# Kernel tuning notes

Measured on AMD Instinct MI355X. Metric: run time of the kernel, lower is better.

The kernel has to match this reference:

```python
import jax, jax.numpy as jnp
import numpy as np

D_IN = 768      # residual-stream width
D_SAE = 16384   # dictionary size
T = 4           # positions per window
K = 64          # TopK sparsity
PREFIX = (8192, 16384)  # prefix_sum for n_scales=2 even split
B = 1024


def setup_inputs() -> dict:
    key = jax.random.key(0)
    ks = jax.random.split(key, 6)
    x = jax.random.normal(ks[0], (B, T, D_IN), jnp.float32)
    # encoder weight ~ kaiming-uniform scale
    W_enc = jax.random.normal(ks[1], (T, D_IN, D_SAE), jnp.float32) * (1.0 / np.sqrt(D_IN))
    b_enc = jnp.zeros((D_SAE,), jnp.float32)
    # per-scale decoders, row-normalized over (T, d_in) as in _normalize_decoder
    def make_dec(k, prefix):
        W = jax.random.normal(k, (prefix, T, D_IN), jnp.float32)
        norms = jnp.linalg.norm(W.reshape(prefix, -1), axis=1).clip(1e-8)
        return W / norms[:, None, None]
    W_dec0 = make_dec(ks[2], PREFIX[0])
    W_dec1 = make_dec(ks[3], PREFIX[1])
    b_dec0 = jnp.zeros((T, D_IN), jnp.float32)
    b_dec1 = jnp.zeros((T, D_IN), jnp.float32)
    # non-identity per-position prefix permutation (T, d_sae)
    perm_keys = jax.random.split(ks[4], T)
    pos_prefix_perm = jax.vmap(lambda k: jax.random.permutation(k, D_SAE))(perm_keys).astype(jnp.int32)
    return {
        'x': x, 'W_enc': W_enc, 'b_enc': b_enc,
        'W_dec0': W_dec0, 'b_dec0': b_dec0,
        'W_dec1': W_dec1, 'b_dec1': b_dec1,
        'pos_prefix_perm': pos_prefix_perm,
    }


def reference(x, W_enc, b_enc, W_dec0, b_dec0, W_dec1, b_dec1, pos_prefix_perm):
    # ---- encode: pre-activation + per-row TopK + ReLU scatter into sparse code z
    pre = jnp.einsum('btd,tds->bs', x, W_enc) + b_enc            # (B, d_sae)
    vals, idx = jax.lax.top_k(pre, K)                            # (B, K)
    b = pre.shape[0]
    z = jnp.zeros_like(pre).at[jnp.arange(b)[:, None], idx].set(jax.nn.relu(vals))
    # ---- matryoshka per-(position, scale) reconstruction loss
    total = jnp.asarray(0.0, pre.dtype)
    x_hat_full = None
    for W, bd in ((W_dec0, b_dec0), (W_dec1, b_dec1)):
        prefix = W.shape[0]
        # position-dependent permutation gather: z_g[b,t,p] = z[b, perm[t,p]]
        z_g = z[:, pos_prefix_perm[:, :prefix]]                  # (B, T, prefix)
        x_hat = jnp.einsum('btp,ptd->btd', z_g, W) + bd          # (B, T, d_in)
        # sum over t of mean_b sum_d err^2  (== loop over t in the original)
        total = total + jnp.sum(jnp.mean(jnp.sum((x_hat - x) ** 2, axis=-1), axis=0))
        x_hat_full = x_hat
    total = total / (T * 2)  # divide by T * n_scales
    # aux-k loss: freshly initialized module has no dead latents
    # (num_tokens_since_fired starts at 0 << dead_threshold_tokens), so l_auxk == 0.
    return total, x_hat_full, z
```

## Files before the change

### kernel.cpp

```cpp
#include <hip/hip_runtime.h>
#include <hip/hip_bf16.h>
#include <stdint.h>

#define NB    1024
#define NT    4
#define NDIN  768
#define NSAE  16384
#define NK    64
#define KDIM  3072
#define PFX0  8192
#define KT96  96
#define VKD   6144

typedef _Float16 f16x8 __attribute__((ext_vector_type(8)));
typedef _Float16 f16x4 __attribute__((ext_vector_type(4)));
typedef float    f32x4 __attribute__((ext_vector_type(4)));

__device__ __forceinline__ unsigned f2key(float f) {
    union { float f; unsigned u; } cv; cv.f = f;
    unsigned u = cv.u;
    return u ^ ((unsigned)((int)u >> 31) | 0x80000000u);
}

__device__ __forceinline__ void ld16(const void* g, void* l) {
    __builtin_amdgcn_global_load_lds(
        (const __attribute__((address_space(1))) void*)g,
        (__attribute__((address_space(3))) void*)l, 16, 0, 0);
}

__global__ __launch_bounds__(256) void conv_a_kernel(
    const float* __restrict__ A, _Float16* __restrict__ A2)
{
    const int gid = blockIdx.x * 256 + threadIdx.x;
    const int m = gid / (KDIM / 4);
    const int k = (gid % (KDIM / 4)) * 4;
    const float4 v = *(const float4*)(A + (size_t)m * KDIM + k);
    const float vv[4] = { v.x, v.y, v.z, v.w };
    f16x4 h, l;
#pragma unroll
    for (int j = 0; j < 4; ++j) {
        const float sv = vv[j] * 64.f;
        const _Float16 hh = (_Float16)sv;
        h[j] = hh;
        l[j] = (_Float16)(sv - (float)hh);
    }
    const size_t ob = (size_t)m * VKD + (k >> 5) * 64 + (k & 31);
    *(f16x4*)(A2 + ob)      = h;
    *(f16x4*)(A2 + ob + 32) = l;
}

__global__ __launch_bounds__(512, 2) void gemm_f16split_kernel(
    const _Float16* __restrict__ A2, const float* __restrict__ Bsrc,
    const float* __restrict__ bias, float* __restrict__ pre)
{
    __shared__ _Float16 sA[2 * 256 * 64];
    __shared__ float    sB32[32 * 256];
    __shared__ _Float16 sBf[256 * 64];
    const int tid = threadIdx.x;
    const int lane = tid & 63;
    const int wid = tid >> 6;
    const int wm = wid >> 2;
    const int wn = wid & 3;

    const int bid = blockIdx.x;
    const int swz = (bid & 7) * 32 + (bid >> 3);
    const int m0 = (swz & 3) * 256;
    const int n0 = (swz >> 2) * 256;

    const _Float16* pa[4]; const float* pb[4];
    _Float16* da[4]; float* db[4];
#pragma unroll
    for (int r = 0; r < 4; ++r) {
        const int d = tid + r * 512;
        const int rowA = d >> 3;
        const int lsA = (d & 7) ^ (rowA & 7);
        pa[r] = A2 + (size_t)(m0 + rowA) * VKD + lsA * 8;
        da[r] = sA + d * 8;
        const int kB = d >> 6;
        const int slotB = d & 63;
        pb[r] = Bsrc + (size_t)kB * NSAE + n0 + slotB * 4;
        db[r] = sB32 + d * 4;
    }

    const int rl = lane & 15;
    const int qw = lane >> 4;
    const int off0 = ((0 + qw) ^ (rl & 7)) * 8 + rl * 64;
    const int off1 = ((4 + qw) ^ (rl & 7)) * 8 + rl * 64;

    const int cvn = tid & 255;
    const int cvkh = tid >> 8;
    const int cvsw = cvn & 7;
    _Float16* const cvout = sBf + cvn * 64;

    f32x4 acc[8][4];
#pragma unroll
    for (int mi = 0; mi < 8; ++mi)
#pragma unroll
        for (int ni = 0; ni < 4; ++ni)
            acc[mi][ni] = (f32x4){0.f, 0.f, 0.f, 0.f};

#pragma unroll
    for (int r = 0; r < 4; ++r) { ld16(pa[r], da[r]); ld16(pb[r], db[r]); }
    asm volatile("s_waitcnt vmcnt(0)" ::: "memory");
    __builtin_amdgcn_sched_barrier(0);
    __builtin_amdgcn_s_barrier();
    __builtin_amdgcn_sched_barrier(0);

    const size_t KSTRB = (size_t)32 * NSAE;

    for (int kt = 0; kt < KT96; ++kt) {
        const int cbA = (kt & 1) ? 16384 : 0;
        const int nbA = cbA ^ 16384;

        {
            float v[16];
#pragma unroll
            for (int j = 0; j < 16; ++j)
                v[j] = sB32[(cvkh * 16 + j) * 256 + cvn];
            f16x8 h0{}, h1{}, l0{}, l1{};
#pragma unroll
            for (int j = 0; j < 8; ++j) {
                const float sv = v[j] * 64.f;
                const _Float16 hh = (_Float16)sv;
                h0[j] = hh;
                l0[j] = (_Float16)(sv - (float)hh);
            }
#pragma unroll
            for (int j = 0; j < 8; ++j) {
                const float sv = v[8 + j] * 64.f;
                const _Float16 hh = (_Float16)sv;
                h1[j] = hh;
                l1[j] = (_Float16)(sv - (float)hh);
            }
            *(f16x8*)(cvout + (((cvkh * 2 + 0) ^ cvsw) * 8)) = h0;
            *(f16x8*)(cvout + (((cvkh * 2 + 1) ^ cvsw) * 8)) = h1;
            *(f16x8*)(cvout + (((4 + cvkh * 2 + 0) ^ cvsw) * 8)) = l0;
            *(f16x8*)(cvout + (((4 + cvkh * 2 + 1) ^ cvsw) * 8)) = l1;
        }
        asm volatile("s_waitcnt lgkmcnt(0)" ::: "memory");
        __builtin_amdgcn_sched_barrier(0);
        __builtin_amdgcn_s_barrier();
        __builtin_amdgcn_sched_barrier(0);

        if (kt + 1 < KT96) {
            const int koA = (kt + 1) * 64;
            const size_t koB = (size_t)(kt + 1) * KSTRB;
#pragma unroll
            for (int r = 0; r < 4; ++r) {
                ld16(pa[r] + koA, da[r] + nbA);
                ld16(pb[r] + koB, db[r]);
            }
        }
        __builtin_amdgcn_s_setprio(1);
        f16x8 bf[4][2];
#pragma unroll
        for (int ni = 0; ni < 4; ++ni) {
            const int rb = (wn * 64 + ni * 16) * 64;
            bf[ni][0] = *(const f16x8*)(sBf + rb + off0);
            bf[ni][1] = *(const f16x8*)(sBf + rb + off1);
        }
#pragma unroll
        for (int h = 0; h < 2; ++h) {
            f16x8 af[4][2];
#pragma unroll
            for (int i = 0; i < 4; ++i) {
                const int ra = cbA + (wm * 128 + (h * 4 + i) * 16) * 64;
                af[i][0] = *(const f16x8*)(sA + ra + off0);
                af[i][1] = *(const f16x8*)(sA + ra + off1);
            }
#pragma unroll
            for (int i = 0; i < 4; ++i)
#pragma unroll
                for (int ni = 0; ni < 4; ++ni) {
                    acc[h * 4 + i][ni] = __builtin_amdgcn_mfma_f32_16x16x32_f16(af[i][0], bf[ni][0], acc[h * 4 + i][ni], 0, 0, 0);
                    acc[h * 4 + i][ni] = __builtin_amdgcn_mfma_f32_16x16x32_f16(af[i][0], bf[ni][1], acc[h * 4 + i][ni], 0, 0, 0);
                    acc[h * 4 + i][ni] = __builtin_amdgcn_mfma_f32_16x16x32_f16(af[i][1], bf[ni][0], acc[h * 4 + i][ni], 0, 0, 0);
                }
        }
        __builtin_amdgcn_s_setprio(0);
        __builtin_amdgcn_sched_barrier(0);
        asm volatile("s_waitcnt vmcnt(0)" ::: "memory");
        __builtin_amdgcn_sched_barrier(0);
        __builtin_amdgcn_s_barrier();
        __builtin_amdgcn_sched_barrier(0);
    }

    const float c12 = 1.0f / 4096.0f;
    float bv[4];
#pragma unroll
    for (int ni = 0; ni < 4; ++ni) bv[ni] = bias[n0 + wn * 64 + ni * 16 + rl];
#pragma unroll
    for (int mi = 0; mi < 8; ++mi)
#pragma unroll
        for (int ni = 0; ni < 4; ++ni)
#pragma unroll
            for (int r = 0; r < 4; ++r) {
                const int row = m0 + wm * 128 + mi * 16 + qw * 4 + r;
                const int col = n0 + wn * 64 + ni * 16 + rl;
                pre[(size_t)row * NSAE + col] = acc[mi][ni][r] * c12 + bv[ni];
            }
}

__global__ __launch_bounds__(256) void gemm_pre_kernel(
    const float* __restrict__ A, const float* __restrict__ Bm,
    const float* __restrict__ bias, float* __restrict__ pre)
{
    __shared__ float As[16][128];
    __shared__ float Bs[16][128];
    const int bn = blockIdx.x * 128;
    const int bm = blockIdx.y * 128;
    const int tid = threadIdx.x;
    const int tx = tid & 15;
    const int ty = tid >> 4;

    float acc[8][8];
#pragma unroll
    for (int i = 0; i < 8; ++i)
#pragma unroll
        for (int j = 0; j < 8; ++j) acc[i][j] = 0.f;

    for (int k0 = 0; k0 < KDIM; k0 += 16) {
#pragma unroll
        for (int i = 0; i < 2; ++i) {
            const int idx = i * 256 + tid;
            const int r = idx >> 2;
            const int c = (idx & 3) << 2;
            const float4 v = *(const float4*)(A + (size_t)(bm + r) * KDIM + (k0 + c));
            As[c + 0][r] = v.x; As[c + 1][r] = v.y;
            As[c + 2][r] = v.z; As[c + 3][r] = v.w;
        }
#pragma unroll
        for (int i = 0; i < 2; ++i) {
            const int idx = i * 256 + tid;
            const int r = idx >> 5;
            const int c = (idx & 31) << 2;
            *(float4*)(&Bs[r][c]) = *(const float4*)(Bm + (size_t)(k0 + r) * NSAE + (bn + c));
        }
        __syncthreads();
#pragma unroll
        for (int kk = 0; kk < 16; ++kk) {
            const float4 a0 = *(const float4*)(&As[kk][ty * 8]);
            const float4 a1 = *(const float4*)(&As[kk][ty * 8 + 4]);
            const float4 b0 = *(const float4*)(&Bs[kk][tx * 8]);
            const float4 b1 = *(const float4*)(&Bs[kk][tx * 8 + 4]);
            const float av[8] = { a0.x, a0.y, a0.z, a0.w, a1.x, a1.y, a1.z, a1.w };
            const float bv[8] = { b0.x, b0.y, b0.z, b0.w, b1.x, b1.y, b1.z, b1.w };
#pragma unroll
            for (int i = 0; i < 8; ++i)
#pragma unroll
                for (int j = 0; j < 8; ++j)
                    acc[i][j] = fmaf(av[i], bv[j], acc[i][j]);
        }
        __syncthreads();
    }

    float bv8[8];
#pragma unroll
    for (int j = 0; j < 8; ++j) bv8[j] = bias[bn + tx * 8 + j];
#pragma unroll
    for (int i = 0; i < 8; ++i) {
        float4 o0, o1;
        o0.x = acc[i][0] + bv8[0]; o0.y = acc[i][1] + bv8[1];
        o0.z = acc[i][2] + bv8[2]; o0.w = acc[i][3] + bv8[3];
        o1.x = acc[i][4] + bv8[4]; o1.y = acc[i][5] + bv8[5];
        o1.z = acc[i][6] + bv8[6]; o1.w = acc[i][7] + bv8[7];
        const size_t off = (size_t)(bm + ty * 8 + i) * NSAE + bn + tx * 8;
        *(float4*)(pre + off) = o0;
        *(float4*)(pre + off + 4) = o1;
    }
}

__global__ __launch_bounds__(256) void topk_kernel(
    const float* __restrict__ pre,
    int* __restrict__ tk_idx, float* __restrict__ tk_val,
    float* __restrict__ z)
{
    __shared__ unsigned hist[4][256];
    __shared__ int sel[NK];
    __shared__ float sval[NK];
    __shared__ int ties[256];
    __shared__ float tval[256];
    __shared__ unsigned sh_prefix, sh_want, sh_cnt, sh_tiecnt;

    const int b = blockIdx.x;
    const int tid = threadIdx.x;
    const int w = tid >> 6;
    const float* row = pre + (size_t)b * NSAE;
    float* zrow = z + (size_t)b * NSAE;

    if (tid == 0) { sh_prefix = 0u; sh_want = NK; sh_cnt = 0u; sh_tiecnt = 0u; }
    hist[0][tid] = 0u; hist[1][tid] = 0u; hist[2][tid] = 0u; hist[3][tid] = 0u;
    __syncthreads();

    float4 rv[16];
#pragma unroll
    for (int j = 0; j < 16; ++j) {
        const int i = tid * 4 + j * 1024;
        rv[j] = *(const float4*)(row + i);
        *(float4*)(zrow + i) = make_float4(0.f, 0.f, 0.f, 0.f);
        atomicAdd(&hist[w][f2key(rv[j].x) >> 24], 1u);
        atomicAdd(&hist[w][f2key(rv[j].y) >> 24], 1u);
        atomicAdd(&hist[w][f2key(rv[j].z) >> 24], 1u);
        atomicAdd(&hist[w][f2key(rv[j].w) >> 24], 1u);
    }
    __syncthreads();
    hist[0][tid] += hist[1][tid] + hist[2][tid] + hist[3][tid];
    __syncthreads();
    if (tid == 0) {
        unsigned cum = 0u; int bsel = 0;
        for (int bin = 255; bin >= 0; --bin) {
            const unsigned c = hist[0][bin];
            if (cum + c >= NK) { bsel = bin; break; }
            cum += c;
        }
        sh_prefix = ((unsigned)bsel << 24);
        sh_want = NK - cum;
    }
    __syncthreads();

    for (int pass = 1; pass < 4; ++pass) {
        hist[0][tid] = 0u; hist[1][tid] = 0u; hist[2][tid] = 0u; hist[3][tid] = 0u;
        __syncthreads();
        const int shift = 24 - pass * 8;
        const unsigned mask = 0xFFFFFFFFu << (shift + 8);
        const unsigned pfx = sh_prefix;
#pragma unroll
        for (int j = 0; j < 16; ++j) {
            const float fv[4] = { rv[j].x, rv[j].y, rv[j].z, rv[j].w };
#pragma unroll
            for (int q = 0; q < 4; ++q) {
                const unsigned k = f2key(fv[q]);
                if ((k & mask) == pfx) atomicAdd(&hist[w][(k >> shift) & 0xFFu], 1u);
            }
        }
        __syncthreads();
        hist[0][tid] += hist[1][tid] + hist[2][tid] + hist[3][tid];
        __syncthreads();
        if (tid == 0) {
            const unsigned want = sh_want;
            unsigned cum = 0u; int bsel = 0;
            for (int bin = 255; bin >= 0; --bin) {
                const unsigned c = hist[0][bin];
                if (cum + c >= want) { bsel = bin; break; }
                cum += c;
            }
            sh_prefix |= ((unsigned)bsel << shift);
            sh_want = want - cum;
        }
        __syncthreads();
    }

    const unsigned T = sh_prefix;
#pragma unroll
    for (int j = 0; j < 16; ++j) {
        const float fv[4] = { rv[j].x, rv[j].y, rv[j].z, rv[j].w };
#pragma unroll
        for (int q = 0; q < 4; ++q) {
            const unsigned k = f2key(fv[q]);
            if (k > T) {
                const unsigned s = atomicAdd(&sh_cnt, 1u);
                sel[s] = tid * 4 + j * 1024 + q;
                sval[s] = fv[q];
            } else if (k == T) {
                const unsigned s = atomicAdd(&sh_tiecnt, 1u);
                if (s < 256u) { ties[s] = tid * 4 + j * 1024 + q; tval[s] = fv[q]; }
            }
        }
    }
    __syncthreads();
    if (tid == 0) {
        const unsigned tc = sh_tiecnt;
        const int n = (int)(tc < 256u ? tc : 256u);
        for (int a = 1; a < n; ++a) {
            const int v = ties[a]; const float fv = tval[a]; int c = a;
            while (c > 0 && ties[c - 1] > v) {
                ties[c] = ties[c - 1]; tval[c] = tval[c - 1]; --c;
            }
            ties[c] = v; tval[c] = fv;
        }
        const int base = (int)sh_cnt;
        const int want = (int)sh_want;
        for (int j = 0; j < want && j < n; ++j) {
            sel[base + j] = ties[j]; sval[base + j] = tval[j];
        }
    }
    __syncthreads();
    if (tid < NK) {
        const int myi = sel[tid];
        int rank = 0;
#pragma unroll 1
        for (int j = 0; j < NK; ++j) rank += (sel[j] < myi) ? 1 : 0;
        const float v = fmaxf(sval[tid], 0.f);
        tk_idx[b * NK + rank] = myi;
        tk_val[b * NK + rank] = v;
        zrow[myi] = v;
    }
}

__global__ __launch_bounds__(256) void invperm_kernel(
    const int* __restrict__ perm, int* __restrict__ ipos)
{
    const int i = blockIdx.x * 256 + threadIdx.x;
    if (i < NT * NSAE) {
        const int t = i >> 14;
        ipos[t * NSAE + perm[i]] = i & (NSAE - 1);
    }
}

__global__ __launch_bounds__(256) void decode_kernel(
    const float* __restrict__ x,
    const int* __restrict__ tk_idx, const float* __restrict__ tk_val,
    const int* __restrict__ ipos,
    const float* __restrict__ Wd0, const float* __restrict__ bd0,
    const float* __restrict__ Wd1, const float* __restrict__ bd1,
    float* __restrict__ xhat, float* __restrict__ part0, float* __restrict__ part1)
{
    const int gbid = blockIdx.x;
    const int t = gbid >> 10;
    const int b = gbid & (NB - 1);
    const int bt = b * NT + t;
    const int tid = threadIdx.x;

    __shared__ int s_p[NK];
    __shared__ float s_v[NK];
    if (tid < NK) {
        const int s = tk_idx[b * NK + tid];
        s_v[tid] = tk_val[b * NK + tid];
        s_p[tid] = ipos[t * NSAE + s];
    }
    __syncthreads();

    float acc0[3], acc1[3];
#pragma unroll
    for (int r = 0; r < 3; ++r) {
        const int d = tid + 256 * r;
        acc0[r] = bd0[t * NDIN + d];
        acc1[r] = bd1[t * NDIN + d];
    }
    for (int j = 0; j < NK; ++j) {
        const int p = s_p[j];
        const float v = s_v[j];
        const float* w1 = Wd1 + ((size_t)p * NT + t) * NDIN;
#pragma unroll
        for (int r = 0; r < 3; ++r) acc1[r] = fmaf(v, w1[tid + 256 * r], acc1[r]);
        if (p < PFX0) {
            const float* w0 = Wd0 + ((size_t)p * NT + t) * NDIN;
#pragma unroll
            for (int r = 0; r < 3; ++r) acc0[r] = fmaf(v, w0[tid + 256 * r], acc0[r]);
        }
    }

    float e0 = 0.f, e1 = 0.f;
#pragma unroll
    for (int r = 0; r < 3; ++r) {
        const int d = tid + 256 * r;
        const float xv = x[(size_t)bt * NDIN + d];
        const float d0 = acc0[r] - xv;
        const float d1 = acc1[r] - xv;
        e0 = fmaf(d0, d0, e0);
        e1 = fmaf(d1, d1, e1);
        xhat[(size_t)bt * NDIN + d] = acc1[r];
    }

    __shared__ float r0[256];
    __shared__ float r1[256];
    r0[tid] = e0; r1[tid] = e1;
    __syncthreads();
    for (int w = 128; w > 0; w >>= 1) {
        if (tid < w) { r0[tid] += r0[tid + w]; r1[tid] += r1[tid + w]; }
        __syncthreads();
    }
    if (tid == 0) { part0[bt] = r0[0]; part1[bt] = r1[0]; }
}

__global__ __launch_bounds__(256) void reduce_kernel(
    const float* __restrict__ part0, const float* __restrict__ part1,
    float* __restrict__ out_total)
{
    __shared__ double red[256];
    const int tid = threadIdx.x;
    double s = 0.0;
    for (int i = tid; i < NB * NT; i += 256)
        s += (double)part0[i] + (double)part1[i];
    red[tid] = s;
    __syncthreads();
    for (int w = 128; w > 0; w >>= 1) {
        if (tid < w) red[tid] += red[tid + w];
        __syncthreads();
    }
    if (tid == 0) out_total[0] = (float)(red[0] / ((double)NB * (double)(NT * 2)));
}

extern "C" void kernel_launch(void* const* d_in, const int* in_sizes, int n_in,
                              void* d_out, int out_size, void* d_ws, size_t ws_size,
                              hipStream_t stream)
{
    const float* x     = (const float*)d_in[0];
    const float* W_enc = (const float*)d_in[1];
    const float* b_enc = (const float*)d_in[2];
    const float* Wd0   = (const float*)d_in[3];
    const float* bd0   = (const float*)d_in[4];
    const float* Wd1   = (const float*)d_in[5];
    const float* bd1   = (const float*)d_in[6];
    const int*   perm  = (const int*)d_in[7];

    float* out       = (float*)d_out;
    float* out_total = out;
    float* out_xhat  = out + 1;
    float* out_z     = out + 1 + (size_t)NB * NT * NDIN;

    char* ws = (char*)d_ws;
    size_t off = 0;
    float* pre = (float*)(ws + off); off += (size_t)NB * NSAE * sizeof(float);

    const size_t szA2 = (size_t)NB * VKD * sizeof(_Float16);
    _Float16* A2 = (_Float16*)(ws + off);
    const size_t off_splits_end = off + szA2;

    const bool fast = (ws_size >= off_splits_end +
        ((size_t)NB * NK * 8 + (size_t)NT * NSAE * 4 + (size_t)NB * NT * 8));
    size_t tail = fast ? off_splits_end : off;
    int*   tk_idx = (int*)(ws + tail);   tail += (size_t)NB * NK * sizeof(int);
    float* tk_val = (float*)(ws + tail); tail += (size_t)NB * NK * sizeof(float);
    int*   ipos   = (int*)(ws + tail);   tail += (size_t)NT * NSAE * sizeof(int);
    float* part0  = (float*)(ws + tail); tail += (size_t)NB * NT * sizeof(float);
    float* part1  = (float*)(ws + tail);

    if (fast) {
        conv_a_kernel<<<(NB * KDIM) / (256 * 4), 256, 0, stream>>>(x, A2);
        gemm_f16split_kernel<<<256, 512, 0, stream>>>(A2, W_enc, b_enc, pre);
    } else {
        gemm_pre_kernel<<<dim3(NSAE / 128, NB / 128), 256, 0, stream>>>(x, W_enc, b_enc, pre);
    }
    invperm_kernel<<<(NT * NSAE) / 256, 256, 0, stream>>>(perm, ipos);
    topk_kernel<<<NB, 256, 0, stream>>>(pre, tk_idx, tk_val, out_z);
    decode_kernel<<<NB * NT, 256, 0, stream>>>(x, tk_idx, tk_val, ipos,
                                               Wd0, bd0, Wd1, bd1,
                                               out_xhat, part0, part1);
    reduce_kernel<<<1, 256, 0, stream>>>(part0, part1, out_total);
}
```

Before: 565.6 us.

## Restructure split-f16 GEMM pipeline: register-staged fragments, double-buffered fp32 B

Each iteration now loads all A and B fragments into registers up front, then reuses single LDS buffers for A and the converted B. The fp32 B staging buffer is double-buffered and prefetched two steps ahead, so the fp32-to-f16 hi/lo conversion for the next step can run alongside this step's MFMAs. The aim is to hide the conversion and global-load latency behind compute. In exchange it holds more fragment registers and drops the occupancy hint from 2 blocks to 1 per CU, which lowers latency hiding across blocks.

```diff
diff --git a/kernel.cpp b/kernel.cpp
--- a/kernel.cpp
+++ b/kernel.cpp
@@ -49,13 +49,13 @@
     *(f16x4*)(A2 + ob + 32) = l;
 }
 
-__global__ __launch_bounds__(512, 2) void gemm_f16split_kernel(
+__global__ __launch_bounds__(512, 1) void gemm_f16split_kernel(
     const _Float16* __restrict__ A2, const float* __restrict__ Bsrc,
     const float* __restrict__ bias, float* __restrict__ pre)
 {
-    __shared__ _Float16 sA[2 * 256 * 64];
-    __shared__ float    sB32[32 * 256];
+    __shared__ _Float16 sA[256 * 64];
     __shared__ _Float16 sBf[256 * 64];
+    __shared__ float    sB32[2 * 32 * 256];
     const int tid = threadIdx.x;
     const int lane = tid & 63;
     const int wid = tid >> 6;
@@ -92,6 +92,34 @@
     const int cvsw = cvn & 7;
     _Float16* const cvout = sBf + cvn * 64;
 
+#define CONVERT(half)                                                         \
+    {                                                                         \
+        const int cvb = (half) * 8192;                                        \
+        float v[16];                                                          \
+        _Pragma("unroll")                                                     \
+        for (int j = 0; j < 16; ++j)                                          \
+            v[j] = sB32[cvb + (cvkh * 16 + j) * 256 + cvn];                   \
+        f16x8 h0{}, h1{}, l0{}, l1{};                                         \
+        _Pragma("unroll")                                                     \
+        for (int j = 0; j < 8; ++j) {                                         \
+            const float sv = v[j] * 64.f;                                     \
+            const _Float16 hh = (_Float16)sv;                                 \
+            h0[j] = hh;                                                       \
+            l0[j] = (_Float16)(sv - (float)hh);                               \
+        }                                                                     \
+        _Pragma("unroll")                                                     \
+        for (int j = 0; j < 8; ++j) {                                         \
+            const float sv = v[8 + j] * 64.f;                                 \
+            const _Float16 hh = (_Float16)sv;                                 \
+            h1[j] = hh;                                                       \
+            l1[j] = (_Float16)(sv - (float)hh);                               \
+        }                                                                     \
+        *(f16x8*)(cvout + (((cvkh * 2 + 0) ^ cvsw) * 8)) = h0;                \
+        *(f16x8*)(cvout + (((cvkh * 2 + 1) ^ cvsw) * 8)) = h1;                \
+        *(f16x8*)(cvout + (((4 + cvkh * 2 + 0) ^ cvsw) * 8)) = l0;            \
+        *(f16x8*)(cvout + (((4 + cvkh * 2 + 1) ^ cvsw) * 8)) = l1;            \
+    }
+
     f32x4 acc[8][4];
 #pragma unroll
     for (int mi = 0; mi < 8; ++mi)
@@ -99,43 +127,37 @@
         for (int ni = 0; ni < 4; ++ni)
             acc[mi][ni] = (f32x4){0.f, 0.f, 0.f, 0.f};
 
-#pragma unroll
-    for (int r = 0; r < 4; ++r) { ld16(pa[r], da[r]); ld16(pb[r], db[r]); }
+    const size_t KSTRB = (size_t)32 * NSAE;
+
+#pragma unroll
+    for (int r = 0; r < 4; ++r) {
+        ld16(pa[r], da[r]);
+        ld16(pb[r], db[r]);
+        ld16(pb[r] + KSTRB, db[r] + 8192);
+    }
     asm volatile("s_waitcnt vmcnt(0)" ::: "memory");
     __builtin_amdgcn_sched_barrier(0);
     __builtin_amdgcn_s_barrier();
     __builtin_amdgcn_sched_barrier(0);
-
-    const size_t KSTRB = (size_t)32 * NSAE;
+    CONVERT(0)
+    asm volatile("s_waitcnt lgkmcnt(0)" ::: "memory");
+    __builtin_amdgcn_sched_barrier(0);
+    __builtin_amdgcn_s_barrier();
+    __builtin_amdgcn_sched_barrier(0);
 
     for (int kt = 0; kt < KT96; ++kt) {
-        const int cbA = (kt & 1) ? 16384 : 0;
-        const int nbA = cbA ^ 16384;
-
-        {
-            float v[16];
-#pragma unroll
-            for (int j = 0; j < 16; ++j)
-                v[j] = sB32[(cvkh * 16 + j) * 256 + cvn];
-            f16x8 h0{}, h1{}, l0{}, l1{};
-#pragma unroll
-            for (int j = 0; j < 8; ++j) {
-                const float sv = v[j] * 64.f;
-                const _Float16 hh = (_Float16)sv;
-                h0[j] = hh;
-                l0[j] = (_Float16)(sv - (float)hh);
-            }
-#pragma unroll
-            for (int j = 0; j < 8; ++j) {
-                const float sv = v[8 + j] * 64.f;
-                const _Float16 hh = (_Float16)sv;
-                h1[j] = hh;
-                l1[j] = (_Float16)(sv - (float)hh);
-            }
-            *(f16x8*)(cvout + (((cvkh * 2 + 0) ^ cvsw) * 8)) = h0;
-            *(f16x8*)(cvout + (((cvkh * 2 + 1) ^ cvsw) * 8)) = h1;
-            *(f16x8*)(cvout + (((4 + cvkh * 2 + 0) ^ cvsw) * 8)) = l0;
-            *(f16x8*)(cvout + (((4 + cvkh * 2 + 1) ^ cvsw) * 8)) = l1;
+        f16x8 af[8][2], bf[4][2];
+#pragma unroll
+        for (int mi = 0; mi < 8; ++mi) {
+            const int ra = (wm * 128 + mi * 16) * 64;
+            af[mi][0] = *(const f16x8*)(sA + ra + off0);
+            af[mi][1] = *(const f16x8*)(sA + ra + off1);
+        }
+#pragma unroll
+        for (int ni = 0; ni < 4; ++ni) {
+            const int rb = (wn * 64 + ni * 16) * 64;
+            bf[ni][0] = *(const f16x8*)(sBf + rb + off0);
+            bf[ni][1] = *(const f16x8*)(sBf + rb + off1);
         }
         asm volatile("s_waitcnt lgkmcnt(0)" ::: "memory");
         __builtin_amdgcn_sched_barrier(0);
@@ -144,46 +166,37 @@
 
         if (kt + 1 < KT96) {
             const int koA = (kt + 1) * 64;
-            const size_t koB = (size_t)(kt + 1) * KSTRB;
-#pragma unroll
-            for (int r = 0; r < 4; ++r) {
-                ld16(pa[r] + koA, da[r] + nbA);
-                ld16(pb[r] + koB, db[r]);
+#pragma unroll
+            for (int r = 0; r < 4; ++r) ld16(pa[r] + koA, da[r]);
+        }
+        if (kt + 2 < KT96) {
+            const size_t koB = (size_t)(kt + 2) * KSTRB;
+            const int bb = (kt & 1) * 8192;
+#pragma unroll
+            for (int r = 0; r < 4; ++r) ld16(pb[r] + koB, db[r] + bb);
+        }
+
+        if (kt + 1 < KT96) CONVERT((kt + 1) & 1)
+
+        __builtin_amdgcn_s_setprio(1);
+#pragma unroll
+        for (int mi = 0; mi < 8; ++mi)
+#pragma unroll
+            for (int ni = 0; ni < 4; ++ni) {
+                acc[mi][ni] = __builtin_amdgcn_mfma_f32_16x16x32_f16(af[mi][0], bf[ni][0], acc[mi][ni], 0, 0, 0);
+                acc[mi][ni] = __builtin_amdgcn_mfma_f32_16x16x32_f16(af[mi][0], bf[ni][1], acc[mi][ni], 0, 0, 0);
+                acc[mi][ni] = __builtin_amdgcn_mfma_f32_16x16x32_f16(af[mi][1], bf[ni][0], acc[mi][ni], 0, 0, 0);
             }
-        }
-        __builtin_amdgcn_s_setprio(1);
-        f16x8 bf[4][2];
-#pragma unroll
-        for (int ni = 0; ni < 4; ++ni) {
-            const int rb = (wn * 64 + ni * 16) * 64;
-            bf[ni][0] = *(const f16x8*)(sBf + rb + off0);
-            bf[ni][1] = *(const f16x8*)(sBf + rb + off1);
-        }
-#pragma unroll
-        for (int h = 0; h < 2; ++h) {
-            f16x8 af[4][2];
-#pragma unroll
-            for (int i = 0; i < 4; ++i) {
-                const int ra = cbA + (wm * 128 + (h * 4 + i) * 16) * 64;
-                af[i][0] = *(const f16x8*)(sA + ra + off0);
-                af[i][1] = *(const f16x8*)(sA + ra + off1);
-            }
-#pragma unroll
-            for (int i = 0; i < 4; ++i)
-#pragma unroll
-                for (int ni = 0; ni < 4; ++ni) {
-                    acc[h * 4 + i][ni] = __builtin_amdgcn_mfma_f32_16x16x32_f16(af[i][0], bf[ni][0], acc[h * 4 + i][ni], 0, 0, 0);
-                    acc[h * 4 + i][ni] = __builtin_amdgcn_mfma_f32_16x16x32_f16(af[i][0], bf[ni][1], acc[h * 4 + i][ni], 0, 0, 0);
-                    acc[h * 4 + i][ni] = __builtin_amdgcn_mfma_f32_16x16x32_f16(af[i][1], bf[ni][0], acc[h * 4 + i][ni], 0, 0, 0);
-                }
-        }
         __builtin_amdgcn_s_setprio(0);
+
         __builtin_amdgcn_sched_barrier(0);
+        asm volatile("s_waitcnt lgkmcnt(0)" ::: "memory");
         asm volatile("s_waitcnt vmcnt(0)" ::: "memory");
         __builtin_amdgcn_sched_barrier(0);
         __builtin_amdgcn_s_barrier();
         __builtin_amdgcn_sched_barrier(0);
     }
+#undef CONVERT
 
     const float c12 = 1.0f / 4096.0f;
     float bv[4];
```

Measured after the change: 853.9 us. +51.0%, slower.

## Compact top-k candidates after first radix pass and parallelize bin selection

Applied to the files above, without the earlier changes.

After the first 8-bit radix histogram, the top-k kernel compacts the elements at or above the selected bin into a shared candidate list (capacity 2048) and runs the remaining radix passes and final selection over that list instead of all 16384 register values. The serial single-thread bin scan is replaced with a parallel suffix scan across 256 threads. It falls back to the full-register path if the candidates overflow. The cost is extra shared memory (about 16KB) and more barriers per pass, which may reduce occupancy. Top-k is only one of several kernels in the pipeline.

```diff
diff --git a/kernel.cpp b/kernel.cpp
--- a/kernel.cpp
+++ b/kernel.cpp
@@ -11,6 +11,7 @@
 #define PFX0  8192
 #define KT96  96
 #define VKD   6144
+#define CCAP  2048
 
 typedef _Float16 f16x8 __attribute__((ext_vector_type(8)));
 typedef _Float16 f16x4 __attribute__((ext_vector_type(4)));
@@ -276,11 +277,14 @@
     float* __restrict__ z)
 {
     __shared__ unsigned hist[4][256];
+    __shared__ unsigned scan[257];
+    __shared__ int   cand[CCAP];
+    __shared__ float cval[CCAP];
     __shared__ int sel[NK];
     __shared__ float sval[NK];
     __shared__ int ties[256];
     __shared__ float tval[256];
-    __shared__ unsigned sh_prefix, sh_want, sh_cnt, sh_tiecnt;
+    __shared__ unsigned sh_prefix, sh_want, sh_cnt, sh_tiecnt, sh_ccnt, sh_bsel;
 
     const int b = blockIdx.x;
     const int tid = threadIdx.x;
@@ -288,7 +292,7 @@
     const float* row = pre + (size_t)b * NSAE;
     float* zrow = z + (size_t)b * NSAE;
 
-    if (tid == 0) { sh_prefix = 0u; sh_want = NK; sh_cnt = 0u; sh_tiecnt = 0u; }
+    if (tid == 0) { sh_cnt = 0u; sh_tiecnt = 0u; sh_ccnt = 0u; }
     hist[0][tid] = 0u; hist[1][tid] = 0u; hist[2][tid] = 0u; hist[3][tid] = 0u;
     __syncthreads();
 
@@ -306,17 +310,43 @@
     __syncthreads();
     hist[0][tid] += hist[1][tid] + hist[2][tid] + hist[3][tid];
     __syncthreads();
-    if (tid == 0) {
-        unsigned cum = 0u; int bsel = 0;
-        for (int bin = 255; bin >= 0; --bin) {
-            const unsigned c = hist[0][bin];
-            if (cum + c >= NK) { bsel = bin; break; }
-            cum += c;
-        }
-        sh_prefix = ((unsigned)bsel << 24);
-        sh_want = NK - cum;
-    }
-    __syncthreads();
+
+    scan[tid] = hist[0][tid];
+    if (tid == 0) scan[256] = 0u;
+    __syncthreads();
+    for (int s = 1; s < 256; s <<= 1) {
+        const unsigned v = (tid + s < 256) ? scan[tid + s] : 0u;
+        __syncthreads();
+        scan[tid] += v;
+        __syncthreads();
+    }
+    if (scan[tid] >= (unsigned)NK && scan[tid + 1] < (unsigned)NK) {
+        sh_bsel = (unsigned)tid;
+        sh_prefix = ((unsigned)tid << 24);
+        sh_want = (unsigned)NK - scan[tid + 1];
+    }
+    __syncthreads();
+    const unsigned bsel0 = sh_bsel;
+
+#pragma unroll
+    for (int j = 0; j < 16; ++j) {
+        const float fv[4] = { rv[j].x, rv[j].y, rv[j].z, rv[j].w };
+#pragma unroll
+        for (int q = 0; q < 4; ++q) {
+            const unsigned k = f2key(fv[q]);
+            if ((k >> 24) >= bsel0) {
+                const unsigned s = atomicAdd(&sh_ccnt, 1u);
+                if (s < (unsigned)CCAP) {
+                    cand[s] = tid * 4 + j * 1024 + q;
+                    cval[s] = fv[q];
+                }
+            }
+        }
+    }
+    __syncthreads();
+    const int ccnt_raw = (int)sh_ccnt;
+    const bool ovf = ccnt_raw > CCAP;
+    const int ccnt = ovf ? 0 : ccnt_raw;
 
     for (int pass = 1; pass < 4; ++pass) {
         hist[0][tid] = 0u; hist[1][tid] = 0u; hist[2][tid] = 0u; hist[3][tid] = 0u;
@@ -324,46 +354,71 @@
         const int shift = 24 - pass * 8;
         const unsigned mask = 0xFFFFFFFFu << (shift + 8);
         const unsigned pfx = sh_prefix;
+        if (!ovf) {
+            for (int i = tid; i < ccnt; i += 256) {
+                const unsigned k = f2key(cval[i]);
+                if ((k & mask) == pfx) atomicAdd(&hist[w][(k >> shift) & 0xFFu], 1u);
+            }
+        } else {
+#pragma unroll
+            for (int j = 0; j < 16; ++j) {
+                const float fv[4] = { rv[j].x, rv[j].y, rv[j].z, rv[j].w };
+#pragma unroll
+                for (int q = 0; q < 4; ++q) {
+                    const unsigned k = f2key(fv[q]);
+                    if ((k & mask) == pfx) atomicAdd(&hist[w][(k >> shift) & 0xFFu], 1u);
+                }
+            }
+        }
+        __syncthreads();
+        hist[0][tid] += hist[1][tid] + hist[2][tid] + hist[3][tid];
+        __syncthreads();
+        scan[tid] = hist[0][tid];
+        if (tid == 0) scan[256] = 0u;
+        __syncthreads();
+        for (int s = 1; s < 256; s <<= 1) {
+            const unsigned v = (tid + s < 256) ? scan[tid + s] : 0u;
+            __syncthreads();
+            scan[tid] += v;
+            __syncthreads();
+        }
+        const unsigned want = sh_want;
+        __syncthreads();
+        if (scan[tid] >= want && scan[tid + 1] < want) {
+            sh_prefix |= ((unsigned)tid << shift);
+            sh_want = want - scan[tid + 1];
+        }
+        __syncthreads();
+    }
+
+    const unsigned T = sh_prefix;
+    if (!ovf) {
+        for (int i = tid; i < ccnt; i += 256) {
+            const unsigned k = f2key(cval[i]);
+            if (k > T) {
+                const unsigned s = atomicAdd(&sh_cnt, 1u);
+                sel[s] = cand[i];
+                sval[s] = cval[i];
+            } else if (k == T) {
+                const unsigned s = atomicAdd(&sh_tiecnt, 1u);
+                if (s < 256u) { ties[s] = cand[i]; tval[s] = cval[i]; }
+            }
+        }
+    } else {
 #pragma unroll
         for (int j = 0; j < 16; ++j) {
             const float fv[4] = { rv[j].x, rv[j].y, rv[j].z, rv[j].w };
 #pragma unroll
             for (int q = 0; q < 4; ++q) {
                 const unsigned k = f2key(fv[q]);
-                if ((k & mask) == pfx) atomicAdd(&hist[w][(k >> shift) & 0xFFu], 1u);
-            }
-        }
-        __syncthreads();
-        hist[0][tid] += hist[1][tid] + hist[2][tid] + hist[3][tid];
-        __syncthreads();
-        if (tid == 0) {
-            const unsigned want = sh_want;
-            unsigned cum = 0u; int bsel = 0;
-            for (int bin = 255; bin >= 0; --bin) {
-                const unsigned c = hist[0][bin];
-                if (cum + c >= want) { bsel = bin; break; }
-                cum += c;
-            }
-            sh_prefix |= ((unsigned)bsel << shift);
-            sh_want = want - cum;
-        }
-        __syncthreads();
-    }
-
-    const unsigned T = sh_prefix;
-#pragma unroll
-    for (int j = 0; j < 16; ++j) {
-        const float fv[4] = { rv[j].x, rv[j].y, rv[j].z, rv[j].w };
-#pragma unroll
-        for (int q = 0; q < 4; ++q) {
-            const unsigned k = f2key(fv[q]);
-            if (k > T) {
-                const unsigned s = atomicAdd(&sh_cnt, 1u);
-                sel[s] = tid * 4 + j * 1024 + q;
-                sval[s] = fv[q];
-            } else if (k == T) {
-                const unsigned s = atomicAdd(&sh_tiecnt, 1u);
-                if (s < 256u) { ties[s] = tid * 4 + j * 1024 + q; tval[s] = fv[q]; }
+                if (k > T) {
+                    const unsigned s = atomicAdd(&sh_cnt, 1u);
+                    sel[s] = tid * 4 + j * 1024 + q;
+                    sval[s] = fv[q];
+                } else if (k == T) {
+                    const unsigned s = atomicAdd(&sh_tiecnt, 1u);
+                    if (s < 256u) { ties[s] = tid * 4 + j * 1024 + q; tval[s] = fv[q]; }
+                }
             }
         }
     }
@@ -466,8 +521,8 @@
     __shared__ float r1[256];
     r0[tid] = e0; r1[tid] = e1;
     __syncthreads();
-    for (int w = 128; w > 0; w >>= 1) {
-        if (tid < w) { r0[tid] += r0[tid + w]; r1[tid] += r1[tid + w]; }
+    for (int w2 = 128; w2 > 0; w2 >>= 1) {
+        if (tid < w2) { r0[tid] += r0[tid + w2]; r1[tid] += r1[tid + w2]; }
         __syncthreads();
     }
     if (tid == 0) { part0[bt] = r0[0]; part1[bt] = r1[0]; }
```

New measurement: 524.7 us (median of 2 runs). -7.2%, faster.
